# Kernel optimization log

Measured on AMD Instinct MI355X. Metric: run time of the kernel, lower is better.

The kernel has to match this reference:

```python
import jax, jax.numpy as jnp
import numpy as np

D_IN = 1024
D_OUT = 1024
N = 4096


def setup_inputs() -> dict:
    key = jax.random.key(0)
    kx, kq, kk, kv = jax.random.split(key, 4)
    s = 1.0 / np.sqrt(D_IN)
    return {
        "x": jax.random.normal(kx, (N, D_IN), dtype=jnp.float32),
        # nn.Linear weights stored as [d_out, d_in]
        "wq": jax.random.uniform(kq, (D_OUT, D_IN), dtype=jnp.float32, minval=-s, maxval=s),
        "wk": jax.random.uniform(kk, (D_OUT, D_IN), dtype=jnp.float32, minval=-s, maxval=s),
        "wv": jax.random.uniform(kv, (D_OUT, D_IN), dtype=jnp.float32, minval=-s, maxval=s),
    }


def reference(x, wq, wk, wv):
    q = x @ wq.T  # [N, d_out]
    k = x @ wk.T
    v = x @ wv.T
    scores = q @ k.T  # [N, N]
    weights = jax.nn.softmax(scores / jnp.sqrt(jnp.asarray(k.shape[-1], x.dtype)), axis=-1)
    return weights @ v  # [N, d_out]
```

## Files before the change

kernel.cpp:

```cpp
#include <hip/hip_runtime.h>
#include <cstdint>

#define NTOK 4096
#define DMODEL 1024

typedef __bf16 bf16x8 __attribute__((ext_vector_type(8)));
typedef float f32x4 __attribute__((ext_vector_type(4)));

__device__ __forceinline__ unsigned short f32_to_bf16(float f) {
    unsigned int u = __float_as_uint(f);
    unsigned int r = 0x7FFFu + ((u >> 16) & 1u);
    return (unsigned short)((u + r) >> 16);
}

__global__ __launch_bounds__(256) void cvt_f32_bf16(const float* __restrict__ in,
                                                    unsigned short* __restrict__ out,
                                                    int n4) {
    int i = blockIdx.x * 256 + threadIdx.x;
    if (i >= n4) return;
    float4 v = reinterpret_cast<const float4*>(in)[i];
    ushort4 o;
    o.x = f32_to_bf16(v.x);
    o.y = f32_to_bf16(v.y);
    o.z = f32_to_bf16(v.z);
    o.w = f32_to_bf16(v.w);
    reinterpret_cast<ushort4*>(out)[i] = o;
}

#define BM 128
#define BN 128
#define BK 64

#define STAGE_TILES(Ablk, lda, Bblk, ldb, k0)                                        \
    _Pragma("unroll") for (int i = 0; i < 4; ++i) {                                  \
        const int c = tid + i * 256;                                                 \
        const int row = c >> 3;                                                      \
        const int jl = (c & 7) ^ (row & 7);                                          \
        const unsigned short* ga = (Ablk) + (size_t)row * (lda) + ((k0) + jl * 8);   \
        const unsigned short* gb = (Bblk) + (size_t)row * (ldb) + ((k0) + jl * 8);   \
        __builtin_amdgcn_global_load_lds(                                            \
            (const __attribute__((address_space(1))) void*)ga,                       \
            (__attribute__((address_space(3))) void*)(&As[c * 8]), 16, 0, 0);        \
        __builtin_amdgcn_global_load_lds(                                            \
            (const __attribute__((address_space(1))) void*)gb,                       \
            (__attribute__((address_space(3))) void*)(&Bs[c * 8]), 16, 0, 0);        \
    }

#define COMPUTE_TILE()                                                               \
    _Pragma("unroll") for (int ks = 0; ks < 2; ++ks) {                               \
        bf16x8 af[4], bfr[4];                                                        \
        _Pragma("unroll") for (int m = 0; m < 4; ++m) {                              \
            const int row = wr * 64 + m * 16 + (lane & 15);                          \
            const int ch = (ks * 4 + (lane >> 4)) ^ (row & 7);                       \
            af[m] = *reinterpret_cast<const bf16x8*>(                                \
                reinterpret_cast<const char*>(As) + row * 128 + ch * 16);            \
        }                                                                            \
        _Pragma("unroll") for (int n = 0; n < 4; ++n) {                              \
            const int row = wc * 64 + n * 16 + (lane & 15);                          \
            const int ch = (ks * 4 + (lane >> 4)) ^ (row & 7);                       \
            bfr[n] = *reinterpret_cast<const bf16x8*>(                               \
                reinterpret_cast<const char*>(Bs) + row * 128 + ch * 16);            \
        }                                                                            \
        _Pragma("unroll") for (int m = 0; m < 4; ++m)                                \
            _Pragma("unroll") for (int n = 0; n < 4; ++n)                            \
                acc[m][n] = __builtin_amdgcn_mfma_f32_16x16x32_bf16(                 \
                    af[m], bfr[n], acc[m][n], 0, 0, 0);                              \
    }

__global__ __launch_bounds__(256, 2) void gemm_nt_f32(
    const unsigned short* __restrict__ A, const unsigned short* __restrict__ B,
    float* __restrict__ C, int K, int lda, int ldb, int ldc) {
    __shared__ __align__(16) unsigned short As[BM * BK];
    __shared__ __align__(16) unsigned short Bs[BN * BK];
    const int tid = threadIdx.x;
    const int lane = tid & 63;
    const int wave = tid >> 6;
    const int wr = wave >> 1, wc = wave & 1;

    const unsigned short* Ablk = A + (size_t)blockIdx.y * BM * lda;
    const unsigned short* Bblk = B + (size_t)blockIdx.x * BN * ldb;
    f32x4 acc[4][4] = {};

    for (int k0 = 0; k0 < K; k0 += BK) {
        STAGE_TILES(Ablk, lda, Bblk, ldb, k0)
        __syncthreads();
        COMPUTE_TILE()
        __syncthreads();
    }

    const int col0 = blockIdx.x * BN + wc * 64 + (lane & 15);
    const int row0 = blockIdx.y * BM + wr * 64 + ((lane >> 4) << 2);
#pragma unroll
    for (int m = 0; m < 4; ++m)
#pragma unroll
        for (int n = 0; n < 4; ++n)
#pragma unroll
            for (int r = 0; r < 4; ++r)
                C[(size_t)(row0 + m * 16 + r) * ldc + (col0 + n * 16)] = acc[m][n][r];
}

__global__ __launch_bounds__(256, 2) void gemm_qkv(
    const unsigned short* __restrict__ xb, const unsigned short* __restrict__ Wb,
    unsigned short* __restrict__ QK, unsigned short* __restrict__ Vt) {
    __shared__ __align__(16) unsigned short As[BM * BK];
    __shared__ __align__(16) unsigned short Bs[BN * BK];
    const int tid = threadIdx.x;
    const int lane = tid & 63;
    const int wave = tid >> 6;
    const int wr = wave >> 1, wc = wave & 1;
    const int bx = blockIdx.x;

    const unsigned short* Ablk = xb + (size_t)blockIdx.y * BM * DMODEL;
    const unsigned short* Bblk = Wb + (size_t)bx * BN * DMODEL;
    f32x4 acc[4][4] = {};

    for (int k0 = 0; k0 < DMODEL; k0 += BK) {
        STAGE_TILES(Ablk, DMODEL, Bblk, DMODEL, k0)
        __syncthreads();
        COMPUTE_TILE()
        __syncthreads();
    }

    const int colw = wc * 64 + (lane & 15);
    const int row0 = blockIdx.y * BM + wr * 64 + ((lane >> 4) << 2);
    if (bx < 16) {
        const int col0 = bx * 128 + colw;
#pragma unroll
        for (int m = 0; m < 4; ++m)
#pragma unroll
            for (int n = 0; n < 4; ++n)
#pragma unroll
                for (int r = 0; r < 4; ++r)
                    QK[(size_t)(row0 + m * 16 + r) * 2048 + (col0 + n * 16)] =
                        f32_to_bf16(acc[m][n][r]);
    } else {
        const int vrow0 = (bx - 16) * 128 + colw;
#pragma unroll
        for (int m = 0; m < 4; ++m)
#pragma unroll
            for (int n = 0; n < 4; ++n) {
                ushort4 o;
                o.x = f32_to_bf16(acc[m][n][0]);
                o.y = f32_to_bf16(acc[m][n][1]);
                o.z = f32_to_bf16(acc[m][n][2]);
                o.w = f32_to_bf16(acc[m][n][3]);
                *reinterpret_cast<ushort4*>(
                    &Vt[(size_t)(vrow0 + n * 16) * NTOK + (row0 + m * 16)]) = o;
            }
    }
}

__global__ __launch_bounds__(256, 2) void gemm_pv_splitk(
    const unsigned short* __restrict__ P, const unsigned short* __restrict__ Vt,
    float* __restrict__ C) {
    __shared__ __align__(16) unsigned short As[BM * BK];
    __shared__ __align__(16) unsigned short Bs[BN * BK];
    const int tid = threadIdx.x;
    const int lane = tid & 63;
    const int wave = tid >> 6;
    const int wr = wave >> 1, wc = wave & 1;

    const unsigned short* Ablk = P + (size_t)blockIdx.y * BM * (2 * NTOK);
    const unsigned short* Bblk = Vt + (size_t)blockIdx.x * BN * NTOK;
    f32x4 acc[4][4] = {};

    const int kbeg = blockIdx.z * (NTOK / 4);
    const int kend = kbeg + NTOK / 4;
    for (int k0 = kbeg; k0 < kend; k0 += BK) {
        STAGE_TILES(Ablk, 2 * NTOK, Bblk, NTOK, k0)
        __syncthreads();
        COMPUTE_TILE()
        __syncthreads();
    }

    const int col0 = blockIdx.x * BN + wc * 64 + (lane & 15);
    const int row0 = blockIdx.y * BM + wr * 64 + ((lane >> 4) << 2);
#pragma unroll
    for (int m = 0; m < 4; ++m)
#pragma unroll
        for (int n = 0; n < 4; ++n)
#pragma unroll
            for (int r = 0; r < 4; ++r)
                unsafeAtomicAdd(&C[(size_t)(row0 + m * 16 + r) * DMODEL + (col0 + n * 16)],
                                acc[m][n][r]);
}

__global__ __launch_bounds__(256) void softmax_rows(float* __restrict__ S, int N) {
    const int row = blockIdx.x;
    float* s = S + (size_t)row * N;
    const int t = threadIdx.x;

    float v[16];
    float mx = -1e30f;
#pragma unroll
    for (int i = 0; i < 4; ++i) {
        float4 x = reinterpret_cast<const float4*>(s)[t + i * 256];
        v[i * 4 + 0] = x.x;
        v[i * 4 + 1] = x.y;
        v[i * 4 + 2] = x.z;
        v[i * 4 + 3] = x.w;
        mx = fmaxf(mx, fmaxf(fmaxf(x.x, x.y), fmaxf(x.z, x.w)));
    }
#pragma unroll
    for (int off = 32; off; off >>= 1) mx = fmaxf(mx, __shfl_xor(mx, off));
    __shared__ float redm[4];
    if (!(t & 63)) redm[t >> 6] = mx;
    __syncthreads();
    mx = fmaxf(fmaxf(redm[0], redm[1]), fmaxf(redm[2], redm[3]));

    float sum = 0.f;
#pragma unroll
    for (int i = 0; i < 16; ++i) {
        v[i] = __expf((v[i] - mx) * 0.03125f);
        sum += v[i];
    }
#pragma unroll
    for (int off = 32; off; off >>= 1) sum += __shfl_xor(sum, off);
    __shared__ float reds[4];
    if (!(t & 63)) reds[t >> 6] = sum;
    __syncthreads();
    sum = (reds[0] + reds[1]) + (reds[2] + reds[3]);
    const float inv = 1.0f / sum;

    unsigned short* p = reinterpret_cast<unsigned short*>(s);
#pragma unroll
    for (int i = 0; i < 4; ++i) {
        ushort4 o;
        o.x = f32_to_bf16(v[i * 4 + 0] * inv);
        o.y = f32_to_bf16(v[i * 4 + 1] * inv);
        o.z = f32_to_bf16(v[i * 4 + 2] * inv);
        o.w = f32_to_bf16(v[i * 4 + 3] * inv);
        reinterpret_cast<ushort4*>(p)[t + i * 256] = o;
    }
}

extern "C" void kernel_launch(void* const* d_in, const int* in_sizes, int n_in,
                              void* d_out, int out_size, void* d_ws, size_t ws_size,
                              hipStream_t stream) {
    (void)in_sizes; (void)n_in; (void)out_size; (void)ws_size;
    const float* x = (const float*)d_in[0];
    const float* wq = (const float*)d_in[1];
    const float* wk = (const float*)d_in[2];
    const float* wv = (const float*)d_in[3];
    float* out = (float*)d_out;

    const size_t MB = 1ull << 20;
    char* w = (char*)d_ws;
    unsigned short* xb = (unsigned short*)(w + 0 * MB);
    unsigned short* Wb = (unsigned short*)(w + 8 * MB);
    unsigned short* QK = (unsigned short*)(w + 14 * MB);
    unsigned short* Vt = (unsigned short*)(w + 30 * MB);
    float* S           = (float*)(w + 38 * MB);

    cvt_f32_bf16<<<4096, 256, 0, stream>>>(x, xb, (NTOK * DMODEL) / 4);
    cvt_f32_bf16<<<1024, 256, 0, stream>>>(wq, Wb, (DMODEL * DMODEL) / 4);
    cvt_f32_bf16<<<1024, 256, 0, stream>>>(wk, Wb + DMODEL * DMODEL, (DMODEL * DMODEL) / 4);
    cvt_f32_bf16<<<1024, 256, 0, stream>>>(wv, Wb + 2 * DMODEL * DMODEL, (DMODEL * DMODEL) / 4);

    gemm_qkv<<<dim3(24, 32), 256, 0, stream>>>(xb, Wb, QK, Vt);

    gemm_nt_f32<<<dim3(32, 32), 256, 0, stream>>>(QK, QK + 1024, S, DMODEL, 2048, 2048, NTOK);

    softmax_rows<<<NTOK, 256, 0, stream>>>(S, NTOK);

    hipMemsetAsync(d_out, 0, (size_t)NTOK * DMODEL * sizeof(float), stream);
    gemm_pv_splitk<<<dim3(8, 32, 4), 256, 0, stream>>>((const unsigned short*)S, Vt, out);
}
```

Measured before the change: 251.4 us.

## Remap GEMM block indices for XCD-aware locality and drop PV split-K

All three GEMMs now launch on a 1D grid and remap block ids so that blocks sharing a group of A row tiles land on the same XCD (id & 7), aiming to improve L2 reuse of shared operand tiles. The PV GEMM no longer splits K four ways with atomic adds. It runs the full K loop per block and writes results directly, which removes the output memset and the atomics. The cost is only 256 blocks for PV, which may underfill the GPU and lengthen the per-block critical path.

After: 229.1 us. 8.8% less time.

```diff
diff --git a/kernel.cpp b/kernel.cpp
--- a/kernel.cpp
+++ b/kernel.cpp
@@ -67,9 +67,8 @@
                     af[m], bfr[n], acc[m][n], 0, 0, 0);                              \
     }
 
-__global__ __launch_bounds__(256, 2) void gemm_nt_f32(
-    const unsigned short* __restrict__ A, const unsigned short* __restrict__ B,
-    float* __restrict__ C, int K, int lda, int ldb, int ldc) {
+__global__ __launch_bounds__(256, 2) void gemm_scores(
+    const unsigned short* __restrict__ QK, float* __restrict__ S) {
     __shared__ __align__(16) unsigned short As[BM * BK];
     __shared__ __align__(16) unsigned short Bs[BN * BK];
     const int tid = threadIdx.x;
@@ -77,26 +76,31 @@
     const int wave = tid >> 6;
     const int wr = wave >> 1, wc = wave & 1;
 
-    const unsigned short* Ablk = A + (size_t)blockIdx.y * BM * lda;
-    const unsigned short* Bblk = B + (size_t)blockIdx.x * BN * ldb;
+    const int id = blockIdx.x;
+    const int g = id & 7, s = id >> 3;
+    const int bx = s >> 2;
+    const int by = (g << 2) + (s & 3);
+
+    const unsigned short* Ablk = QK + (size_t)by * BM * 2048;
+    const unsigned short* Bblk = QK + 1024 + (size_t)bx * BN * 2048;
     f32x4 acc[4][4] = {};
 
-    for (int k0 = 0; k0 < K; k0 += BK) {
-        STAGE_TILES(Ablk, lda, Bblk, ldb, k0)
+    for (int k0 = 0; k0 < DMODEL; k0 += BK) {
+        STAGE_TILES(Ablk, 2048, Bblk, 2048, k0)
         __syncthreads();
         COMPUTE_TILE()
         __syncthreads();
     }
 
-    const int col0 = blockIdx.x * BN + wc * 64 + (lane & 15);
-    const int row0 = blockIdx.y * BM + wr * 64 + ((lane >> 4) << 2);
+    const int col0 = bx * BN + wc * 64 + (lane & 15);
+    const int row0 = by * BM + wr * 64 + ((lane >> 4) << 2);
 #pragma unroll
     for (int m = 0; m < 4; ++m)
 #pragma unroll
         for (int n = 0; n < 4; ++n)
 #pragma unroll
             for (int r = 0; r < 4; ++r)
-                C[(size_t)(row0 + m * 16 + r) * ldc + (col0 + n * 16)] = acc[m][n][r];
+                S[(size_t)(row0 + m * 16 + r) * NTOK + (col0 + n * 16)] = acc[m][n][r];
 }
 
 __global__ __launch_bounds__(256, 2) void gemm_qkv(
@@ -108,9 +112,13 @@
     const int lane = tid & 63;
     const int wave = tid >> 6;
     const int wr = wave >> 1, wc = wave & 1;
-    const int bx = blockIdx.x;
-
-    const unsigned short* Ablk = xb + (size_t)blockIdx.y * BM * DMODEL;
+
+    const int id = blockIdx.x;
+    const int g = id & 7, s = id >> 3;
+    const int bx = s % 24;
+    const int by = (g << 2) + s / 24;
+
+    const unsigned short* Ablk = xb + (size_t)by * BM * DMODEL;
     const unsigned short* Bblk = Wb + (size_t)bx * BN * DMODEL;
     f32x4 acc[4][4] = {};
 
@@ -122,7 +130,7 @@
     }
 
     const int colw = wc * 64 + (lane & 15);
-    const int row0 = blockIdx.y * BM + wr * 64 + ((lane >> 4) << 2);
+    const int row0 = by * BM + wr * 64 + ((lane >> 4) << 2);
     if (bx < 16) {
         const int col0 = bx * 128 + colw;
 #pragma unroll
@@ -150,7 +158,7 @@
     }
 }
 
-__global__ __launch_bounds__(256, 2) void gemm_pv_splitk(
+__global__ __launch_bounds__(256, 2) void gemm_pv(
     const unsigned short* __restrict__ P, const unsigned short* __restrict__ Vt,
     float* __restrict__ C) {
     __shared__ __align__(16) unsigned short As[BM * BK];
@@ -160,29 +168,31 @@
     const int wave = tid >> 6;
     const int wr = wave >> 1, wc = wave & 1;
 
-    const unsigned short* Ablk = P + (size_t)blockIdx.y * BM * (2 * NTOK);
-    const unsigned short* Bblk = Vt + (size_t)blockIdx.x * BN * NTOK;
+    const int id = blockIdx.x;
+    const int g = id & 7, s = id >> 3;
+    const int bx = s & 7;
+    const int by = (g << 2) + (s >> 3);
+
+    const unsigned short* Ablk = P + (size_t)by * BM * (2 * NTOK);
+    const unsigned short* Bblk = Vt + (size_t)bx * BN * NTOK;
     f32x4 acc[4][4] = {};
 
-    const int kbeg = blockIdx.z * (NTOK / 4);
-    const int kend = kbeg + NTOK / 4;
-    for (int k0 = kbeg; k0 < kend; k0 += BK) {
+    for (int k0 = 0; k0 < NTOK; k0 += BK) {
         STAGE_TILES(Ablk, 2 * NTOK, Bblk, NTOK, k0)
         __syncthreads();
         COMPUTE_TILE()
         __syncthreads();
     }
 
-    const int col0 = blockIdx.x * BN + wc * 64 + (lane & 15);
-    const int row0 = blockIdx.y * BM + wr * 64 + ((lane >> 4) << 2);
+    const int col0 = bx * BN + wc * 64 + (lane & 15);
+    const int row0 = by * BM + wr * 64 + ((lane >> 4) << 2);
 #pragma unroll
     for (int m = 0; m < 4; ++m)
 #pragma unroll
         for (int n = 0; n < 4; ++n)
 #pragma unroll
             for (int r = 0; r < 4; ++r)
-                unsafeAtomicAdd(&C[(size_t)(row0 + m * 16 + r) * DMODEL + (col0 + n * 16)],
-                                acc[m][n][r]);
+                C[(size_t)(row0 + m * 16 + r) * DMODEL + (col0 + n * 16)] = acc[m][n][r];
 }
 
 __global__ __launch_bounds__(256) void softmax_rows(float* __restrict__ S, int N) {
@@ -257,12 +267,11 @@
     cvt_f32_bf16<<<1024, 256, 0, stream>>>(wk, Wb + DMODEL * DMODEL, (DMODEL * DMODEL) / 4);
     cvt_f32_bf16<<<1024, 256, 0, stream>>>(wv, Wb + 2 * DMODEL * DMODEL, (DMODEL * DMODEL) / 4);
 
-    gemm_qkv<<<dim3(24, 32), 256, 0, stream>>>(xb, Wb, QK, Vt);
-
-    gemm_nt_f32<<<dim3(32, 32), 256, 0, stream>>>(QK, QK + 1024, S, DMODEL, 2048, 2048, NTOK);
+    gemm_qkv<<<768, 256, 0, stream>>>(xb, Wb, QK, Vt);
+
+    gemm_scores<<<1024, 256, 0, stream>>>(QK, S);
 
     softmax_rows<<<NTOK, 256, 0, stream>>>(S, NTOK);
 
-    hipMemsetAsync(d_out, 0, (size_t)NTOK * DMODEL * sizeof(float), stream);
-    gemm_pv_splitk<<<dim3(8, 32, 4), 256, 0, stream>>>((const unsigned short*)S, Vt, out);
-}
+    gemm_pv<<<256, 256, 0, stream>>>((const unsigned short*)S, Vt, out);
+}
```
